# Performance work log

Measured on AMD Instinct MI355X. Metric: run time of the kernel, lower is better.

The kernel has to match this reference:

```python
import jax, jax.numpy as jnp
import numpy as np

VOCAB = 1000
EMB = 64
HID = 64


def _lstm_last(x, mask, Wx, Wh, b):
    """Keras-style LSTM over time, returning final hidden state.

    x:    [T, B, EMB] float
    mask: [T, B] bool  (False = padded step: state carried through, Keras mask_zero semantics)
    Wx:   [EMB, 4H], Wh: [H, 4H], b: [4H]; gate order i, f, g(c), o.
    """
    T, B, _ = x.shape
    h0 = jnp.zeros((B, HID), x.dtype)
    c0 = jnp.zeros((B, HID), x.dtype)

    def step(carry, inp):
        h, c = carry
        x_t, m_t = inp
        z = x_t @ Wx + h @ Wh + b                      # [B, 4H]
        i, f, g, o = jnp.split(z, 4, axis=-1)
        i = jax.nn.sigmoid(i)
        f = jax.nn.sigmoid(f)
        o = jax.nn.sigmoid(o)
        c_new = f * c + i * jnp.tanh(g)
        h_new = o * jnp.tanh(c_new)
        m = m_t[:, None]
        h = jnp.where(m, h_new, h)
        c = jnp.where(m, c_new, c)
        return (h, c), None

    (h_T, _), _ = jax.lax.scan(step, (h0, c0), (x, mask))
    return h_T


def setup_inputs() -> dict:
    key = jax.random.key(0)
    ks = jax.random.split(key, 8)
    B, T = 512, 1024
    tokens = jax.random.randint(ks[0], (B, T), 0, VOCAB, dtype=jnp.int32)
    emb_table = jax.random.normal(ks[1], (VOCAB, EMB), jnp.float32) * 0.05
    def glorot(k, shape):
        lim = np.sqrt(6.0 / (shape[0] + shape[1]))
        return jax.random.uniform(k, shape, jnp.float32, -lim, lim)
    # Keras unit_forget_bias: bias of forget gate initialized to 1.
    b_init = jnp.concatenate([jnp.zeros(HID), jnp.ones(HID), jnp.zeros(2 * HID)]).astype(jnp.float32)
    return {
        "tokens": tokens,
        "emb_table": emb_table,
        "Wx_f": glorot(ks[2], (EMB, 4 * HID)),
        "Wh_f": glorot(ks[3], (HID, 4 * HID)),
        "b_f": b_init,
        "Wx_b": glorot(ks[4], (EMB, 4 * HID)),
        "Wh_b": glorot(ks[5], (HID, 4 * HID)),
        "b_b": b_init,
    }


def reference(tokens, emb_table, Wx_f, Wh_f, b_f, Wx_b, Wh_b, b_b):
    # Embedding with mask_zero=True: token 0 is masked.
    emb = emb_table[tokens]                  # [B, T, EMB]
    mask = tokens != 0                       # [B, T]
    x = jnp.transpose(emb, (1, 0, 2))        # [T, B, EMB]
    m = jnp.transpose(mask, (1, 0))          # [T, B]
    h_fwd = _lstm_last(x, m, Wx_f, Wh_f, b_f)
    # Backward direction: Keras go_backwards reverses the sequence (and mask).
    h_bwd = _lstm_last(x[::-1], m[::-1], Wx_b, Wh_b, b_b)
    return jnp.concatenate([h_fwd, h_bwd], axis=-1)  # [B, 2H]
```

## Files before the change

kernel.cpp:

```cpp
#include <hip/hip_runtime.h>

#define T_STEPS 1024
#define B_TOT   512
#define VOCAB   1000
#define EMB     64
#define HID     64
#define GATES   256

typedef float f4 __attribute__((ext_vector_type(4)));
typedef float f2 __attribute__((ext_vector_type(2)));

__device__ __forceinline__ float fast_rcp(float x)  { return __builtin_amdgcn_rcpf(x); }
__device__ __forceinline__ float fast_exp2(float x) { return __builtin_amdgcn_exp2f(x); }

__device__ __forceinline__ float sigmoid_f(float x) {
    return fast_rcp(1.0f + fast_exp2(-1.4426950408889634f * x));
}
__device__ __forceinline__ float tanh_f(float x) {
    float e = fast_exp2(2.8853900817779268f * x);
    return 1.0f - 2.0f * fast_rcp(e + 1.0f);
}

__device__ __forceinline__ void pk_fma_acc(f2& acc, f2 a, f2 b) {
    asm("v_pk_fma_f32 %0, %1, %2, %0" : "+v"(acc) : "v"(a), "v"(b));
}

__global__ __launch_bounds__(256, 4)
void zx_table_kernel(const float* __restrict__ emb,
                     const float* __restrict__ Wx_f, const float* __restrict__ b_f,
                     const float* __restrict__ Wx_b, const float* __restrict__ b_b,
                     float* __restrict__ zx_tab)
{
    const int bid = blockIdx.x;
    const int dir = bid / VOCAB;
    const int v   = bid - dir * VOCAB;
    const int j   = threadIdx.x;
    const int p   = j & 1;
    const int u   = (j >> 1) & 63;
    const int w   = j >> 7;
    const int col = (2 * w + p) * HID + u;

    const float* __restrict__ Wx = dir ? Wx_b : Wx_f;
    const float* __restrict__ bv = dir ? b_b  : b_f;

    __shared__ float4 x4[EMB / 4];
    if (j < EMB / 4) x4[j] = ((const float4*)emb)[v * (EMB / 4) + j];
    __syncthreads();

    float a0 = bv[col], a1 = 0.f, a2 = 0.f, a3 = 0.f;
#pragma unroll
    for (int q = 0; q < EMB / 4; ++q) {
        float4 xv = x4[q];
        a0 = fmaf(xv.x, Wx[(4 * q + 0) * GATES + col], a0);
        a1 = fmaf(xv.y, Wx[(4 * q + 1) * GATES + col], a1);
        a2 = fmaf(xv.z, Wx[(4 * q + 2) * GATES + col], a2);
        a3 = fmaf(xv.w, Wx[(4 * q + 3) * GATES + col], a3);
    }
    zx_tab[(dir * VOCAB + v) * GATES + j] = (a0 + a1) + (a2 + a3);
}

__global__ __launch_bounds__(128, 2)
void lstm_rec_kernel(const int* __restrict__ tokens,
                     const float* __restrict__ Wh_f,
                     const float* __restrict__ Wh_b,
                     const float* __restrict__ zx_tab,
                     float* __restrict__ out)
{
    const int bx  = blockIdx.x;
    const int dir = bx >> 9;
    const int row = bx & 511;
    const int u   = threadIdx.x & 63;
    const int w   = threadIdx.x >> 6;

    const float* __restrict__ Wh   = dir ? Wh_b : Wh_f;
    const f2*    __restrict__ zx2  = (const f2*)(zx_tab + dir * (VOCAB * GATES));
    const int*   __restrict__ trow = tokens + row * T_STEPS;

    const int colA = (2 * w) * HID + u;
    const int colB = colA + HID;
    f2 whA2[HID / 2], whB2[HID / 2];
#pragma unroll
    for (int m = 0; m < HID / 2; ++m) {
        f2 a; a.x = Wh[(2 * m) * GATES + colA]; a.y = Wh[(2 * m + 1) * GATES + colA];
        whA2[m] = a;
        f2 b; b.x = Wh[(2 * m) * GATES + colB]; b.y = Wh[(2 * m + 1) * GATES + colB];
        whB2[m] = b;
    }

    __shared__ float hbuf[HID];
    __shared__ f2    act2[HID];

    if (threadIdx.x < HID) hbuf[threadIdx.x] = 0.0f;
    float c = 0.0f;
    __syncthreads();

    int tokc = trow[dir ? (T_STEPS - 1) : 0];
    int tokn = trow[dir ? (T_STEPS - 2) : 1];
    f2  zxc  = zx2[tokc * 128 + w * 64 + u];

    const f4* __restrict__ hb4 = (const f4*)hbuf;

#pragma unroll 2
    for (int t = 0; t < T_STEPS; ++t) {
        int t2   = (t + 2 < T_STEPS) ? (t + 2) : (T_STEPS - 1);
        int tokf = trow[dir ? (T_STEPS - 1 - t2) : t2];
        f2  zxn  = zx2[tokn * 128 + w * 64 + u];

        __builtin_amdgcn_s_setprio(1);
        f2 accA0; accA0.x = zxc.x; accA0.y = 0.f;
        f2 accA1; accA1.x = 0.f;   accA1.y = 0.f;
        f2 accB0; accB0.x = zxc.y; accB0.y = 0.f;
        f2 accB1; accB1.x = 0.f;   accB1.y = 0.f;
#pragma unroll
        for (int q = 0; q < HID / 4; ++q) {
            f4 hv = hb4[q];
            f2 hlo; hlo.x = hv.x; hlo.y = hv.y;
            f2 hhi; hhi.x = hv.z; hhi.y = hv.w;
            pk_fma_acc(accA0, hlo, whA2[2 * q]);
            pk_fma_acc(accA1, hhi, whA2[2 * q + 1]);
            pk_fma_acc(accB0, hlo, whB2[2 * q]);
            pk_fma_acc(accB1, hhi, whB2[2 * q + 1]);
        }
        __builtin_amdgcn_s_setprio(0);
        float zA = (accA0.x + accA1.x) + (accA0.y + accA1.y);
        float zB = (accB0.x + accB1.x) + (accB0.y + accB1.y);

        float actA, actB;
        if (w == 0) {
            actA = sigmoid_f(zA);
            actB = sigmoid_f(zB);
        } else {
            actA = tanh_f(zA);
            actB = sigmoid_f(zB);
            f2 go; go.x = actA; go.y = actB;
            act2[u] = go;
        }
        __syncthreads();

        if (w == 0) {
            f2 go = act2[u];
            float c_new = fmaf(actB, c, actA * go.x);
            float h_new = go.y * tanh_f(c_new);
            bool m = (tokc != 0);
            c = m ? c_new : c;
            hbuf[u] = m ? h_new : hbuf[u];
        }
        __syncthreads();

        tokc = tokn; tokn = tokf; zxc = zxn;
    }

    if (w == 0)
        out[row * (2 * HID) + dir * HID + u] = hbuf[u];
}

extern "C" void kernel_launch(void* const* d_in, const int* in_sizes, int n_in,
                              void* d_out, int out_size, void* d_ws, size_t ws_size,
                              hipStream_t stream) {
    const int*   tokens = (const int*)  d_in[0];
    const float* emb    = (const float*)d_in[1];
    const float* Wx_f   = (const float*)d_in[2];
    const float* Wh_f   = (const float*)d_in[3];
    const float* b_f    = (const float*)d_in[4];
    const float* Wx_b   = (const float*)d_in[5];
    const float* Wh_b   = (const float*)d_in[6];
    const float* b_b    = (const float*)d_in[7];
    float* out = (float*)d_out;

    float* zx_tab = (float*)d_ws;

    hipLaunchKernelGGL(zx_table_kernel, dim3(2 * VOCAB), dim3(GATES), 0, stream,
                       emb, Wx_f, b_f, Wx_b, b_b, zx_tab);
    hipLaunchKernelGGL(lstm_rec_kernel, dim3(2 * B_TOT), dim3(128), 0, stream,
                       tokens, Wh_f, Wh_b, zx_tab, out);
}
```

Baseline: 575.2 us.

## Exchange gates via lane shuffles with double-buffered h, one barrier per step

Remaps threads so each wave holds both gate halves for 32 hidden units: lanes 0-31 compute i/f gates and lanes 32-63 compute g/o gates, and they swap values with __shfl_xor instead of going through shared memory. The tanh branch is folded into a scaled sigmoid so all lanes run the same instructions. The hidden state is double-buffered in LDS, which removes the second __syncthreads per timestep and spreads the cell update across all 128 threads. Both halves redundantly compute the c/h update, and the tanh-via-sigmoid identity adds a little arithmetic.

Measured after the change: 566.7 us. No clear change (-1.5%).

```diff
diff --git a/kernel.cpp b/kernel.cpp
--- a/kernel.cpp
+++ b/kernel.cpp
@@ -66,17 +66,19 @@
                      const float* __restrict__ zx_tab,
                      float* __restrict__ out)
 {
-    const int bx  = blockIdx.x;
-    const int dir = bx >> 9;
-    const int row = bx & 511;
-    const int u   = threadIdx.x & 63;
-    const int w   = threadIdx.x >> 6;
+    const int bx   = blockIdx.x;
+    const int dir  = bx >> 9;
+    const int row  = bx & 511;
+    const int l    = threadIdx.x & 63;
+    const int w    = threadIdx.x >> 6;
+    const int half = l >> 5;
+    const int u    = w * 32 + (l & 31);
 
     const float* __restrict__ Wh   = dir ? Wh_b : Wh_f;
     const f2*    __restrict__ zx2  = (const f2*)(zx_tab + dir * (VOCAB * GATES));
     const int*   __restrict__ trow = tokens + row * T_STEPS;
 
-    const int colA = (2 * w) * HID + u;
+    const int colA = (2 * half) * HID + u;
     const int colB = colA + HID;
     f2 whA2[HID / 2], whB2[HID / 2];
 #pragma unroll
@@ -87,24 +89,28 @@
         whB2[m] = b;
     }
 
-    __shared__ float hbuf[HID];
-    __shared__ f2    act2[HID];
+    const float kin  = half ? 2.0f : 1.0f;
+    const float kmul = half ? 2.0f : 1.0f;
+    const float kadd = half ? -1.0f : 0.0f;
 
-    if (threadIdx.x < HID) hbuf[threadIdx.x] = 0.0f;
-    float c = 0.0f;
+    __shared__ float hb[2][HID];
+
+    if (threadIdx.x < HID) { hb[0][threadIdx.x] = 0.0f; hb[1][threadIdx.x] = 0.0f; }
+    float c = 0.0f, h = 0.0f;
+    int   p = 0;
     __syncthreads();
 
     int tokc = trow[dir ? (T_STEPS - 1) : 0];
     int tokn = trow[dir ? (T_STEPS - 2) : 1];
-    f2  zxc  = zx2[tokc * 128 + w * 64 + u];
-
-    const f4* __restrict__ hb4 = (const f4*)hbuf;
+    f2  zxc  = zx2[tokc * 128 + half * 64 + u];
 
 #pragma unroll 2
     for (int t = 0; t < T_STEPS; ++t) {
         int t2   = (t + 2 < T_STEPS) ? (t + 2) : (T_STEPS - 1);
         int tokf = trow[dir ? (T_STEPS - 1 - t2) : t2];
-        f2  zxn  = zx2[tokn * 128 + w * 64 + u];
+        f2  zxn  = zx2[tokn * 128 + half * 64 + u];
+
+        const f4* __restrict__ hb4 = (const f4*)&hb[p][0];
 
         __builtin_amdgcn_s_setprio(1);
         f2 accA0; accA0.x = zxc.x; accA0.y = 0.f;
@@ -125,33 +131,31 @@
         float zA = (accA0.x + accA1.x) + (accA0.y + accA1.y);
         float zB = (accB0.x + accB1.x) + (accB0.y + accB1.y);
 
-        float actA, actB;
-        if (w == 0) {
-            actA = sigmoid_f(zA);
-            actB = sigmoid_f(zB);
-        } else {
-            actA = tanh_f(zA);
-            actB = sigmoid_f(zB);
-            f2 go; go.x = actA; go.y = actB;
-            act2[u] = go;
-        }
+        float actA = fmaf(kmul, sigmoid_f(kin * zA), kadd);
+        float actB = sigmoid_f(zB);
+
+        float othA = __shfl_xor(actA, 32);
+        float othB = __shfl_xor(actB, 32);
+
+        float ig = half ? othA : actA;
+        float fg = half ? othB : actB;
+        float gg = half ? actA : othA;
+        float og = half ? actB : othB;
+        float c_new = fmaf(fg, c, ig * gg);
+        float h_new = og * tanh_f(c_new);
+        bool  m = (tokc != 0);
+        c = m ? c_new : c;
+        h = m ? h_new : h;
+
+        hb[p ^ 1][u] = h;
         __syncthreads();
-
-        if (w == 0) {
-            f2 go = act2[u];
-            float c_new = fmaf(actB, c, actA * go.x);
-            float h_new = go.y * tanh_f(c_new);
-            bool m = (tokc != 0);
-            c = m ? c_new : c;
-            hbuf[u] = m ? h_new : hbuf[u];
-        }
-        __syncthreads();
+        p ^= 1;
 
         tokc = tokn; tokn = tokf; zxc = zxn;
     }
 
-    if (w == 0)
-        out[row * (2 * HID) + dir * HID + u] = hbuf[u];
+    if (!half)
+        out[row * (2 * HID) + dir * HID + u] = h;
 }
 
 extern "C" void kernel_launch(void* const* d_in, const int* in_sizes, int n_in,
```
